# Performance work log

Measured on AMD Instinct MI355X. Metric: run time of the kernel, lower is better.

Reference implementation:

```python
import jax, jax.numpy as jnp
import numpy as np

B, N, ITERS = 8, 4096, 10  # batch, neurons (self.size), async-update sweeps


def setup_inputs() -> dict:
    key = jax.random.key(0)
    k1, k2, k3 = jax.random.split(key, 3)
    # bipolar {-1,+1} query patterns
    x = jnp.sign(jax.random.normal(k1, (B, N), dtype=jnp.float32))
    x = jnp.where(x == 0, 1.0, x)
    # symmetric Hebbian-style weight matrix with zero diagonal (as produced by fit())
    A = jax.random.normal(k2, (N, N), dtype=jnp.float32) / N
    W = 0.5 * (A + A.T)
    W = W - jnp.diag(jnp.diag(W))
    # one random neuron-visit permutation per (sample, sweep), replacing random.shuffle
    perm_keys = jax.random.split(k3, B * ITERS)
    perms = jax.vmap(lambda k: jax.random.permutation(k, N))(perm_keys)
    perms = perms.reshape(B, ITERS, N).astype(jnp.int32)
    return {"x": x, "weights": W, "perms": perms}


def reference(x, weights, perms):
    """Asynchronous Hopfield update: for each sample, sweep ITERS times over a
    random permutation of neurons, setting y[i] = sign(W[i] . y) sequentially."""
    flat_perms = perms.reshape(perms.shape[0], -1)  # [B, ITERS*N]

    def single(y0, perm_flat):
        def step(y, i):
            z = jnp.dot(weights[i], y)  # length-N dot, depends on previous updates
            return y.at[i].set(jnp.sign(z)), None
        y, _ = jax.lax.scan(step, y0, perm_flat)
        return y

    return jax.vmap(single)(x, flat_perms)  # [B, N]
```

## Files before the change

kernel.cpp:

```cpp
#include <hip/hip_runtime.h>

#define N 4096
#define B 8
#define ITERS 10
#define T (ITERS * N)
#define NT 256
#define E 16
#define WIN 1024
#define INFK 0xFFFFFFFFu
#define LIMIT 0x01000000u

__device__ __forceinline__ void lds_barrier() {
    asm volatile("s_waitcnt lgkmcnt(0)\n\ts_barrier" ::: "memory");
}

__global__ __launch_bounds__(256) void z0_gemv(const float* __restrict__ W,
                                               const float* __restrict__ x,
                                               double* __restrict__ Z0) {
    const int i = blockIdx.x;
    const int tid = threadIdx.x;
    const int lane = tid & 63;
    const int wid = tid >> 6;
    const float4* __restrict__ row = (const float4*)(W + (size_t)i * N);
    const float4* __restrict__ xv = (const float4*)x;

    double acc[B];
#pragma unroll
    for (int b = 0; b < B; ++b) acc[b] = 0.0;

#pragma unroll
    for (int it = 0; it < 4; ++it) {
        const int c = tid + 256 * it;
        const float4 w = row[c];
#pragma unroll
        for (int b = 0; b < B; ++b) {
            const float4 xb = xv[b * (N / 4) + c];
            acc[b] += (double)w.x * (double)xb.x + (double)w.y * (double)xb.y +
                      (double)w.z * (double)xb.z + (double)w.w * (double)xb.w;
        }
    }

#pragma unroll
    for (int off = 32; off > 0; off >>= 1) {
#pragma unroll
        for (int b = 0; b < B; ++b) acc[b] += __shfl_down(acc[b], off, 64);
    }

    __shared__ double red[4][B];
    if (lane == 0) {
#pragma unroll
        for (int b = 0; b < B; ++b) red[wid][b] = acc[b];
    }
    __syncthreads();
    if (tid < B)
        Z0[(size_t)tid * N + i] = red[0][tid] + red[1][tid] + red[2][tid] + red[3][tid];
}

__device__ __forceinline__ unsigned umin2(unsigned a, unsigned b) { return a < b ? a : b; }

template <int CTRL>
__device__ __forceinline__ unsigned dpp_min(unsigned v) {
    const int t = __builtin_amdgcn_update_dpp((int)v, (int)v, CTRL, 0xF, 0xF, false);
    return umin2(v, (unsigned)t);
}

__device__ __forceinline__ unsigned wave_min64(unsigned v) {
    v = dpp_min<0x111>(v);
    v = dpp_min<0x112>(v);
    v = dpp_min<0x114>(v);
    v = dpp_min<0x118>(v);
    v = dpp_min<0x142>(v);
    v = dpp_min<0x143>(v);
    return (unsigned)__builtin_amdgcn_readlane((int)v, 63);
}

__device__ __forceinline__ void fetch_row(const float* __restrict__ W, int i,
                                          int tid, float* wr) {
    const float4* __restrict__ rp = (const float4*)(W + (size_t)i * N) + 4 * tid;
    const float4 a = rp[0], c = rp[1], e = rp[2], f = rp[3];
    wr[0] = a.x;  wr[1] = a.y;  wr[2] = a.z;  wr[3] = a.w;
    wr[4] = c.x;  wr[5] = c.y;  wr[6] = c.z;  wr[7] = c.w;
    wr[8] = e.x;  wr[9] = e.y;  wr[10] = e.z; wr[11] = e.w;
    wr[12] = f.x; wr[13] = f.y; wr[14] = f.z; wr[15] = f.w;
}

__global__ __launch_bounds__(256) void hop_seq(const float* __restrict__ W,
                                               const float* __restrict__ x,
                                               const int* __restrict__ perms,
                                               const double* __restrict__ Z0,
                                               float* __restrict__ out) {
    const int b = blockIdx.x;
    const int tid = threadIdx.x;
    const int wid = tid >> 6;
    const int lane = tid & 63;

    __shared__ int wpos[N];
    __shared__ __align__(16) unsigned aP1[2][4];
    __shared__ __align__(16) unsigned aP2[2][4];
    __shared__ __align__(16) unsigned aV[2][4];

    double zj[E], zm[E];
    unsigned ym[E];
    unsigned sk[E];
    {
        const double* __restrict__ zsrc = Z0 + (size_t)b * N + E * tid;
#pragma unroll
        for (int k = 0; k < E; ++k) zj[k] = zsrc[k];
        const float4* __restrict__ xs = (const float4*)(x + (size_t)b * N);
#pragma unroll
        for (int q = 0; q < 4; ++q) {
            const float4 xv = xs[4 * tid + q];
            ym[4 * q + 0] = (xv.x > 0.f) ? 0xFFFFFFFFu : 0x7FFFFFFFu;
            ym[4 * q + 1] = (xv.y > 0.f) ? 0xFFFFFFFFu : 0x7FFFFFFFu;
            ym[4 * q + 2] = (xv.z > 0.f) ? 0xFFFFFFFFu : 0x7FFFFFFFu;
            ym[4 * q + 3] = (xv.w > 0.f) ? 0xFFFFFFFFu : 0x7FFFFFFFu;
        }
    }
    {
        const int4 z4 = make_int4(0, 0, 0, 0);
#pragma unroll
        for (int q = 0; q < 4; ++q) ((int4*)wpos)[tid + 256 * q] = z4;
    }
    lds_barrier();

    const int* __restrict__ perm_b = perms + (size_t)b * T;
    unsigned r = 0;

    for (int base = 0; base < T; base += WIN) {
        const int epoch = (base >> 10) + 1;
        const int4 iv = ((const int4*)(perm_b + base))[tid];
        wpos[iv.x] = (epoch << 10) | (4 * tid + 0);
        wpos[iv.y] = (epoch << 10) | (4 * tid + 1);
        wpos[iv.z] = (epoch << 10) | (4 * tid + 2);
        wpos[iv.w] = (epoch << 10) | (4 * tid + 3);
        lds_barrier();
#pragma unroll
        for (int q = 0; q < 4; ++q) {
            const int4 wp = ((const int4*)wpos)[4 * tid + q];
            const int e0 = 4 * q;
            const unsigned i0 = (unsigned)(E * tid + e0);
            sk[e0 + 0] = ((wp.x >> 10) == epoch)
                ? (((unsigned)(wp.x & 1023) << 14) | ((i0 + 0) << 2) | ((ym[e0 + 0] >> 30) & 2u)) : INFK;
            sk[e0 + 1] = ((wp.y >> 10) == epoch)
                ? (((unsigned)(wp.y & 1023) << 14) | ((i0 + 1) << 2) | ((ym[e0 + 1] >> 30) & 2u)) : INFK;
            sk[e0 + 2] = ((wp.z >> 10) == epoch)
                ? (((unsigned)(wp.z & 1023) << 14) | ((i0 + 2) << 2) | ((ym[e0 + 2] >> 30) & 2u)) : INFK;
            sk[e0 + 3] = ((wp.w >> 10) == epoch)
                ? (((unsigned)(wp.w & 1023) << 14) | ((i0 + 3) << 2) | ((ym[e0 + 3] >> 30) & 2u)) : INFK;
        }

        unsigned f1 = 0, f2v = 0;
        unsigned awk1 = 0, awk2 = 0;
        unsigned ckR = 0;
        float w1[E], w2[E];

        for (;;) {
            unsigned ckP, ckM = 0, gspan = 0;
            int i1 = 0, i2 = 0;
            double d1 = 0.0, d2 = 0.0;
            if (f1) {
                i1 = (int)((awk1 >> 2) & 4095u);
                d1 = (double)(-2 * ((int)(awk1 & 3u) - 1));
                if (f2v) {
                    i2 = (int)((awk2 >> 2) & 4095u);
                    d2 = (double)(-2 * ((int)(awk2 & 3u) - 1));
                    ckM = ((awk1 >> 14) + 1u) << 14;
                    ckP = ((awk2 >> 14) + 1u) << 14;
                    gspan = ckP - ckM;
                    if (tid == (i2 >> 4)) {
                        const int kk = i2 & 15;
#pragma unroll
                        for (int k = 0; k < E; ++k)
                            if (k == kk) { ym[k] ^= 0x80000000u; sk[k] ^= 2u; }
                    }
                } else {
                    ckP = ((awk1 >> 14) + 1u) << 14;
                }
                if (tid == (i1 >> 4)) {
                    const int kk = i1 & 15;
#pragma unroll
                    for (int k = 0; k < E; ++k)
                        if (k == kk) { ym[k] ^= 0x80000000u; sk[k] ^= 2u; }
                }
            } else {
                ckP = ckR;
            }

            unsigned keyP = INFK, vmin = INFK;
            if (f2v) {
#pragma unroll
                for (int k = 0; k < E; ++k) {
                    const double a = fma(d1, (double)w1[k], zj[k]);
                    zm[k] = a;
                    const unsigned tm = ((unsigned)__double2hiint(a)) ^ ym[k];
                    const unsigned cM = sk[k] | (unsigned)(((int)tm) >> 31);
                    vmin = umin2(vmin, cM - ckM);
                    const double c = fma(d2, (double)w2[k], a);
                    zj[k] = c;
                    const unsigned tp = ((unsigned)__double2hiint(c)) ^ ym[k];
                    keyP = umin2(keyP, (sk[k] | (unsigned)(((int)tp) >> 31)) - ckP);
                }
            } else if (f1) {
#pragma unroll
                for (int k = 0; k < E; ++k) {
                    const double c = fma(d1, (double)w1[k], zj[k]);
                    zj[k] = c;
                    const unsigned tp = ((unsigned)__double2hiint(c)) ^ ym[k];
                    keyP = umin2(keyP, (sk[k] | (unsigned)(((int)tp) >> 31)) - ckP);
                }
            } else {
#pragma unroll
                for (int k = 0; k < E; ++k) {
                    const unsigned tp = ((unsigned)__double2hiint(zj[k])) ^ ym[k];
                    keyP = umin2(keyP, (sk[k] | (unsigned)(((int)tp) >> 31)) - ckP);
                }
            }

            const unsigned m1 = wave_min64(keyP);
            const unsigned mv = f2v ? wave_min64(vmin) : INFK;
            const unsigned m2 = wave_min64(keyP == m1 ? INFK : keyP);

            const unsigned p = r & 1u; ++r;
            if (lane == 0) { aP1[p][wid] = m1; aP2[p][wid] = m2; aV[p][wid] = mv; }
            lds_barrier();
            const uint4 P1 = *(const uint4*)&aP1[p][0];
            const unsigned gP = umin2(umin2(P1.x, P1.y), umin2(P1.z, P1.w));
            if (f2v) {
                const uint4 V4 = *(const uint4*)&aV[p][0];
                const unsigned gV = umin2(umin2(V4.x, V4.y), umin2(V4.z, V4.w));
                if (gV < gspan) {
#pragma unroll
                    for (int k = 0; k < E; ++k) zj[k] = zm[k];
                    if (tid == (i2 >> 4)) {
                        const int kk = i2 & 15;
#pragma unroll
                        for (int k = 0; k < E; ++k)
                            if (k == kk) { ym[k] ^= 0x80000000u; sk[k] ^= 2u; }
                    }
                    const unsigned vabs = gV + ckM;
                    if ((vabs >> 14) == (awk2 >> 14)) {
                        f1 = 0; f2v = 0; ckR = ckM;
                    } else {
                        awk1 = vabs; f1 = 1; f2v = 0;
                        fetch_row(W, (int)((awk1 >> 2) & 4095u), tid, w1);
                    }
                    continue;
                }
            }
            if (gP >= LIMIT) break;
            awk1 = gP + ckP; f1 = 1;
            fetch_row(W, (int)((awk1 >> 2) & 4095u), tid, w1);
            const uint4 P2 = *(const uint4*)&aP2[p][0];
            const unsigned o0 = (P1.x == gP) ? P2.x : P1.x;
            const unsigned o1 = (P1.y == gP) ? P2.y : P1.y;
            const unsigned o2 = (P1.z == gP) ? P2.z : P1.z;
            const unsigned o3 = (P1.w == gP) ? P2.w : P1.w;
            const unsigned gP2 = umin2(umin2(o0, o1), umin2(o2, o3));
            f2v = (gP2 < LIMIT) ? 1u : 0u;
            if (f2v) {
                awk2 = gP2 + ckP;
                fetch_row(W, (int)((awk2 >> 2) & 4095u), tid, w2);
            }
        }
    }

    float4* __restrict__ os = (float4*)(out + (size_t)b * N);
#pragma unroll
    for (int q = 0; q < 4; ++q) {
        float4 o;
        o.x = (ym[4 * q + 0] & 0x80000000u) ? 1.0f : -1.0f;
        o.y = (ym[4 * q + 1] & 0x80000000u) ? 1.0f : -1.0f;
        o.z = (ym[4 * q + 2] & 0x80000000u) ? 1.0f : -1.0f;
        o.w = (ym[4 * q + 3] & 0x80000000u) ? 1.0f : -1.0f;
        os[4 * tid + q] = o;
    }
}

extern "C" void kernel_launch(void* const* d_in, const int* in_sizes, int n_in,
                              void* d_out, int out_size, void* d_ws, size_t ws_size,
                              hipStream_t stream) {
    const float* x = (const float*)d_in[0];
    const float* W = (const float*)d_in[1];
    const int* perms = (const int*)d_in[2];
    float* out = (float*)d_out;
    double* Z0 = (double*)d_ws;

    hipLaunchKernelGGL(z0_gemv, dim3(N), dim3(256), 0, stream, W, x, Z0);
    hipLaunchKernelGGL(hop_seq, dim3(B), dim3(NT), 0, stream, W, x, perms, Z0, out);
}
```

Baseline: 2.324 ms.

## Deepen speculative flip batching from two to four candidates per barrier round

Each barrier round now takes up to four lowest-key flip candidates instead of two. It applies their row updates in sequence and validates each speculative step with extra wave-min reductions, rolling back to the first point where an earlier neuron would flip. The aim is to cut the number of block-wide barrier and reduction rounds in the sequential async sweep. The cost is more row fetches, more FMA work and more reductions per round, higher register pressure (two extra weight rows held in registers), and wasted work when speculation fails.

After: 2.640 ms. +13.6%, slower.

```diff
diff --git a/kernel.cpp b/kernel.cpp
--- a/kernel.cpp
+++ b/kernel.cpp
@@ -57,6 +57,9 @@
 }
 
 __device__ __forceinline__ unsigned umin2(unsigned a, unsigned b) { return a < b ? a : b; }
+__device__ __forceinline__ unsigned umin4(unsigned a, unsigned b, unsigned c, unsigned d) {
+    return umin2(umin2(a, b), umin2(c, d));
+}
 
 template <int CTRL>
 __device__ __forceinline__ unsigned dpp_min(unsigned v) {
@@ -84,22 +87,31 @@
     wr[12] = f.x; wr[13] = f.y; wr[14] = f.z; wr[15] = f.w;
 }
 
-__global__ __launch_bounds__(256) void hop_seq(const float* __restrict__ W,
-                                               const float* __restrict__ x,
-                                               const int* __restrict__ perms,
-                                               const double* __restrict__ Z0,
-                                               float* __restrict__ out) {
+#define FIXUP(ii)                                                         \
+    do {                                                                  \
+        if (tid == ((ii) >> 4)) {                                         \
+            const int kk = (ii) & 15;                                     \
+            _Pragma("unroll") for (int k = 0; k < E; ++k) if (k == kk) {  \
+                ym[k] ^= 0x80000000u;                                     \
+                sk[k] ^= 2u;                                              \
+            }                                                             \
+        }                                                                 \
+    } while (0)
+
+__global__ __launch_bounds__(256, 1) void hop_seq(const float* __restrict__ W,
+                                                  const float* __restrict__ x,
+                                                  const int* __restrict__ perms,
+                                                  const double* __restrict__ Z0,
+                                                  float* __restrict__ out) {
     const int b = blockIdx.x;
     const int tid = threadIdx.x;
     const int wid = tid >> 6;
     const int lane = tid & 63;
 
     __shared__ int wpos[N];
-    __shared__ __align__(16) unsigned aP1[2][4];
-    __shared__ __align__(16) unsigned aP2[2][4];
-    __shared__ __align__(16) unsigned aV[2][4];
-
-    double zj[E], zm[E];
+    __shared__ __align__(16) unsigned pub[2][5][4];
+
+    double zj[E], zc[E];
     unsigned ym[E];
     unsigned sk[E];
     {
@@ -149,117 +161,198 @@
                 ? (((unsigned)(wp.w & 1023) << 14) | ((i0 + 3) << 2) | ((ym[e0 + 3] >> 30) & 2u)) : INFK;
         }
 
-        unsigned f1 = 0, f2v = 0;
-        unsigned awk1 = 0, awk2 = 0;
+        unsigned n = 0;
+        unsigned wk1 = 0, wk2 = 0, wk3 = 0, wk4 = 0;
         unsigned ckR = 0;
-        float w1[E], w2[E];
+        float w1[E], w2[E], w3[E], w4[E];
 
         for (;;) {
-            unsigned ckP, ckM = 0, gspan = 0;
-            int i1 = 0, i2 = 0;
-            double d1 = 0.0, d2 = 0.0;
-            if (f1) {
-                i1 = (int)((awk1 >> 2) & 4095u);
-                d1 = (double)(-2 * ((int)(awk1 & 3u) - 1));
-                if (f2v) {
-                    i2 = (int)((awk2 >> 2) & 4095u);
-                    d2 = (double)(-2 * ((int)(awk2 & 3u) - 1));
-                    ckM = ((awk1 >> 14) + 1u) << 14;
-                    ckP = ((awk2 >> 14) + 1u) << 14;
-                    gspan = ckP - ckM;
-                    if (tid == (i2 >> 4)) {
-                        const int kk = i2 & 15;
-#pragma unroll
-                        for (int k = 0; k < E; ++k)
-                            if (k == kk) { ym[k] ^= 0x80000000u; sk[k] ^= 2u; }
-                    }
-                } else {
-                    ckP = ((awk1 >> 14) + 1u) << 14;
-                }
-                if (tid == (i1 >> 4)) {
-                    const int kk = i1 & 15;
-#pragma unroll
-                    for (int k = 0; k < E; ++k)
-                        if (k == kk) { ym[k] ^= 0x80000000u; sk[k] ^= 2u; }
+            unsigned ck1 = 0, ck2 = 0, ck3 = 0, ck4 = 0, ckP;
+            int i1 = 0, i2 = 0, i3 = 0, i4 = 0;
+            double d1 = 0.0, d2 = 0.0, d3 = 0.0, d4 = 0.0;
+            if (n >= 1) {
+                i1 = (int)((wk1 >> 2) & 4095u);
+                d1 = (double)(-2 * ((int)(wk1 & 3u) - 1));
+                ck1 = ((wk1 >> 14) + 1u) << 14;
+                FIXUP(i1);
+            }
+            if (n >= 2) {
+                i2 = (int)((wk2 >> 2) & 4095u);
+                d2 = (double)(-2 * ((int)(wk2 & 3u) - 1));
+                ck2 = ((wk2 >> 14) + 1u) << 14;
+                FIXUP(i2);
+            }
+            if (n >= 3) {
+                i3 = (int)((wk3 >> 2) & 4095u);
+                d3 = (double)(-2 * ((int)(wk3 & 3u) - 1));
+                ck3 = ((wk3 >> 14) + 1u) << 14;
+                FIXUP(i3);
+            }
+            if (n >= 4) {
+                i4 = (int)((wk4 >> 2) & 4095u);
+                d4 = (double)(-2 * ((int)(wk4 & 3u) - 1));
+                ck4 = ((wk4 >> 14) + 1u) << 14;
+                FIXUP(i4);
+            }
+            ckP = (n == 0) ? ckR : (n == 1) ? ck1 : (n == 2) ? ck2 : (n == 3) ? ck3 : ck4;
+
+            unsigned key1 = INFK, key2 = INFK, key3 = INFK, keyP = INFK;
+            if (n == 0) {
+#pragma unroll
+                for (int k = 0; k < E; ++k) {
+                    const unsigned t = ((unsigned)__double2hiint(zj[k])) ^ ym[k];
+                    keyP = umin2(keyP, (sk[k] | (unsigned)(((int)t) >> 31)) - ckR);
                 }
             } else {
-                ckP = ckR;
-            }
-
-            unsigned keyP = INFK, vmin = INFK;
-            if (f2v) {
 #pragma unroll
                 for (int k = 0; k < E; ++k) {
                     const double a = fma(d1, (double)w1[k], zj[k]);
-                    zm[k] = a;
-                    const unsigned tm = ((unsigned)__double2hiint(a)) ^ ym[k];
-                    const unsigned cM = sk[k] | (unsigned)(((int)tm) >> 31);
-                    vmin = umin2(vmin, cM - ckM);
-                    const double c = fma(d2, (double)w2[k], a);
-                    zj[k] = c;
-                    const unsigned tp = ((unsigned)__double2hiint(c)) ^ ym[k];
-                    keyP = umin2(keyP, (sk[k] | (unsigned)(((int)tp) >> 31)) - ckP);
-                }
-            } else if (f1) {
-#pragma unroll
-                for (int k = 0; k < E; ++k) {
-                    const double c = fma(d1, (double)w1[k], zj[k]);
-                    zj[k] = c;
-                    const unsigned tp = ((unsigned)__double2hiint(c)) ^ ym[k];
-                    keyP = umin2(keyP, (sk[k] | (unsigned)(((int)tp) >> 31)) - ckP);
-                }
-            } else {
-#pragma unroll
-                for (int k = 0; k < E; ++k) {
-                    const unsigned tp = ((unsigned)__double2hiint(zj[k])) ^ ym[k];
-                    keyP = umin2(keyP, (sk[k] | (unsigned)(((int)tp) >> 31)) - ckP);
+                    zc[k] = a;
+                    const unsigned t = ((unsigned)__double2hiint(a)) ^ ym[k];
+                    key1 = umin2(key1, (sk[k] | (unsigned)(((int)t) >> 31)) - ck1);
+                }
+                if (n == 1) {
+#pragma unroll
+                    for (int k = 0; k < E; ++k) zj[k] = zc[k];
+                    keyP = key1;
+                }
+                if (n >= 2) {
+#pragma unroll
+                    for (int k = 0; k < E; ++k) {
+                        const double c = fma(d2, (double)w2[k], zc[k]);
+                        zj[k] = c;
+                        const unsigned t = ((unsigned)__double2hiint(c)) ^ ym[k];
+                        key2 = umin2(key2, (sk[k] | (unsigned)(((int)t) >> 31)) - ck2);
+                    }
+                    if (n == 2) keyP = key2;
+                }
+                if (n >= 3) {
+#pragma unroll
+                    for (int k = 0; k < E; ++k) {
+                        const double c = fma(d3, (double)w3[k], zj[k]);
+                        zj[k] = c;
+                        const unsigned t = ((unsigned)__double2hiint(c)) ^ ym[k];
+                        key3 = umin2(key3, (sk[k] | (unsigned)(((int)t) >> 31)) - ck3);
+                    }
+                    if (n == 3) keyP = key3;
+                }
+                if (n >= 4) {
+                    unsigned key4 = INFK;
+#pragma unroll
+                    for (int k = 0; k < E; ++k) {
+                        const double c = fma(d4, (double)w4[k], zj[k]);
+                        zj[k] = c;
+                        const unsigned t = ((unsigned)__double2hiint(c)) ^ ym[k];
+                        key4 = umin2(key4, (sk[k] | (unsigned)(((int)t) >> 31)) - ck4);
+                    }
+                    keyP = key4;
                 }
             }
 
             const unsigned m1 = wave_min64(keyP);
-            const unsigned mv = f2v ? wave_min64(vmin) : INFK;
+            const unsigned mv1 = (n >= 2) ? wave_min64(key1) : INFK;
+            const unsigned mv2 = (n >= 3) ? wave_min64(key2) : INFK;
+            const unsigned mv3 = (n >= 4) ? wave_min64(key3) : INFK;
             const unsigned m2 = wave_min64(keyP == m1 ? INFK : keyP);
 
+            unsigned pv = m1;
+            pv = (lane == 1) ? m2 : pv;
+            pv = (lane == 2) ? mv1 : pv;
+            pv = (lane == 3) ? mv2 : pv;
+            pv = (lane == 4) ? mv3 : pv;
             const unsigned p = r & 1u; ++r;
-            if (lane == 0) { aP1[p][wid] = m1; aP2[p][wid] = m2; aV[p][wid] = mv; }
+            if (lane < 5) pub[p][lane][wid] = pv;
             lds_barrier();
-            const uint4 P1 = *(const uint4*)&aP1[p][0];
-            const unsigned gP = umin2(umin2(P1.x, P1.y), umin2(P1.z, P1.w));
-            if (f2v) {
-                const uint4 V4 = *(const uint4*)&aV[p][0];
-                const unsigned gV = umin2(umin2(V4.x, V4.y), umin2(V4.z, V4.w));
-                if (gV < gspan) {
-#pragma unroll
-                    for (int k = 0; k < E; ++k) zj[k] = zm[k];
-                    if (tid == (i2 >> 4)) {
-                        const int kk = i2 & 15;
-#pragma unroll
-                        for (int k = 0; k < E; ++k)
-                            if (k == kk) { ym[k] ^= 0x80000000u; sk[k] ^= 2u; }
+
+            const uint4 M1 = *(const uint4*)&pub[p][0][0];
+            const uint4 M2 = *(const uint4*)&pub[p][1][0];
+
+            if (n >= 2) {
+                const uint4 V1 = *(const uint4*)&pub[p][2][0];
+                const unsigned gv1 = umin4(V1.x, V1.y, V1.z, V1.w);
+                if (gv1 < ck2 - ck1) {
+#pragma unroll
+                    for (int k = 0; k < E; ++k) zj[k] = zc[k];
+                    FIXUP(i2);
+                    if (n >= 3) FIXUP(i3);
+                    if (n >= 4) FIXUP(i4);
+                    const unsigned vabs = gv1 + ck1;
+                    if ((vabs >> 14) == (wk2 >> 14)) { n = 0; ckR = ck2; }
+                    else { wk1 = vabs; n = 1; fetch_row(W, (int)((vabs >> 2) & 4095u), tid, w1); }
+                    continue;
+                }
+            }
+            if (n >= 3) {
+                const uint4 V2 = *(const uint4*)&pub[p][3][0];
+                const unsigned gv2 = umin4(V2.x, V2.y, V2.z, V2.w);
+                if (gv2 < ck3 - ck2) {
+#pragma unroll
+                    for (int k = 0; k < E; ++k) zj[k] = fma(d2, (double)w2[k], zc[k]);
+                    FIXUP(i3);
+                    if (n >= 4) FIXUP(i4);
+                    const unsigned vabs = gv2 + ck2;
+                    if ((vabs >> 14) == (wk3 >> 14)) { n = 0; ckR = ck3; }
+                    else { wk1 = vabs; n = 1; fetch_row(W, (int)((vabs >> 2) & 4095u), tid, w1); }
+                    continue;
+                }
+            }
+            if (n >= 4) {
+                const uint4 V3 = *(const uint4*)&pub[p][4][0];
+                const unsigned gv3 = umin4(V3.x, V3.y, V3.z, V3.w);
+                if (gv3 < ck4 - ck3) {
+#pragma unroll
+                    for (int k = 0; k < E; ++k)
+                        zj[k] = fma(d3, (double)w3[k], fma(d2, (double)w2[k], zc[k]));
+                    FIXUP(i4);
+                    const unsigned vabs = gv3 + ck3;
+                    if ((vabs >> 14) == (wk4 >> 14)) { n = 0; ckR = ck4; }
+                    else { wk1 = vabs; n = 1; fetch_row(W, (int)((vabs >> 2) & 4095u), tid, w1); }
+                    continue;
+                }
+            }
+
+            unsigned h0 = M1.x, h1 = M1.y, h2 = M1.z, h3 = M1.w;
+            unsigned x0 = M2.x, x1 = M2.y, x2 = M2.z, x3 = M2.w;
+            const unsigned g1 = umin4(h0, h1, h2, h3);
+            if (g1 >= LIMIT) break;
+            {
+                const bool c0 = (h0 == g1), c1 = (h1 == g1), c2 = (h2 == g1), c3 = (h3 == g1);
+                h0 = c0 ? x0 : h0; x0 = c0 ? INFK : x0;
+                h1 = c1 ? x1 : h1; x1 = c1 ? INFK : x1;
+                h2 = c2 ? x2 : h2; x2 = c2 ? INFK : x2;
+                h3 = c3 ? x3 : h3; x3 = c3 ? INFK : x3;
+            }
+            const unsigned g2 = umin4(h0, h1, h2, h3);
+            {
+                const bool c0 = (h0 == g2), c1 = (h1 == g2), c2 = (h2 == g2), c3 = (h3 == g2);
+                h0 = c0 ? x0 : h0; x0 = c0 ? INFK : x0;
+                h1 = c1 ? x1 : h1; x1 = c1 ? INFK : x1;
+                h2 = c2 ? x2 : h2; x2 = c2 ? INFK : x2;
+                h3 = c3 ? x3 : h3; x3 = c3 ? INFK : x3;
+            }
+            const unsigned g3 = umin4(h0, h1, h2, h3);
+            {
+                const bool c0 = (h0 == g3), c1 = (h1 == g3), c2 = (h2 == g3), c3 = (h3 == g3);
+                h0 = c0 ? x0 : h0;
+                h1 = c1 ? x1 : h1;
+                h2 = c2 ? x2 : h2;
+                h3 = c3 ? x3 : h3;
+            }
+            const unsigned g4 = umin4(h0, h1, h2, h3);
+
+            wk1 = g1 + ckP; n = 1;
+            fetch_row(W, (int)((wk1 >> 2) & 4095u), tid, w1);
+            if (g2 < LIMIT) {
+                wk2 = g2 + ckP; n = 2;
+                fetch_row(W, (int)((wk2 >> 2) & 4095u), tid, w2);
+                if (g3 < LIMIT) {
+                    wk3 = g3 + ckP; n = 3;
+                    fetch_row(W, (int)((wk3 >> 2) & 4095u), tid, w3);
+                    if (g4 < LIMIT) {
+                        wk4 = g4 + ckP; n = 4;
+                        fetch_row(W, (int)((wk4 >> 2) & 4095u), tid, w4);
                     }
-                    const unsigned vabs = gV + ckM;
-                    if ((vabs >> 14) == (awk2 >> 14)) {
-                        f1 = 0; f2v = 0; ckR = ckM;
-                    } else {
-                        awk1 = vabs; f1 = 1; f2v = 0;
-                        fetch_row(W, (int)((awk1 >> 2) & 4095u), tid, w1);
-                    }
-                    continue;
-                }
-            }
-            if (gP >= LIMIT) break;
-            awk1 = gP + ckP; f1 = 1;
-            fetch_row(W, (int)((awk1 >> 2) & 4095u), tid, w1);
-            const uint4 P2 = *(const uint4*)&aP2[p][0];
-            const unsigned o0 = (P1.x == gP) ? P2.x : P1.x;
-            const unsigned o1 = (P1.y == gP) ? P2.y : P1.y;
-            const unsigned o2 = (P1.z == gP) ? P2.z : P1.z;
-            const unsigned o3 = (P1.w == gP) ? P2.w : P1.w;
-            const unsigned gP2 = umin2(umin2(o0, o1), umin2(o2, o3));
-            f2v = (gP2 < LIMIT) ? 1u : 0u;
-            if (f2v) {
-                awk2 = gP2 + ckP;
-                fetch_row(W, (int)((awk2 >> 2) & 4095u), tid, w2);
+                }
             }
         }
     }
```

## Replace triple wave-min reductions with quarter-wave DPP mins and speculative row prefetch

Applied to the files above, without the earlier changes.

The per-step reduction is reworked. The three full wave reductions (min, second-min, validation) become one 16-lane quarter-wave DPP min published as 16 LDS candidates plus one full-wave min for validation, which drops the readlane calls. The first-min and second-min are then derived from the 16 published values, and the next row fetch is issued before the validation check is resolved. The z0_gemv kernel is also changed to process two rows per block, reusing each x load, and hop_seq gets launch_bounds(256,1). The goal is to shorten the serial critical path of each sequential update step, at the cost of some wasted speculative fetches.

Result: faster. 2.216 ms (-4.6%).

```diff
diff --git a/kernel.cpp b/kernel.cpp
--- a/kernel.cpp
+++ b/kernel.cpp
@@ -17,46 +17,60 @@
 __global__ __launch_bounds__(256) void z0_gemv(const float* __restrict__ W,
                                                const float* __restrict__ x,
                                                double* __restrict__ Z0) {
-    const int i = blockIdx.x;
+    const int i0 = 2 * blockIdx.x;
     const int tid = threadIdx.x;
     const int lane = tid & 63;
     const int wid = tid >> 6;
-    const float4* __restrict__ row = (const float4*)(W + (size_t)i * N);
+    const float4* __restrict__ row0 = (const float4*)(W + (size_t)i0 * N);
+    const float4* __restrict__ row1 = (const float4*)(W + (size_t)(i0 + 1) * N);
     const float4* __restrict__ xv = (const float4*)x;
 
-    double acc[B];
-#pragma unroll
-    for (int b = 0; b < B; ++b) acc[b] = 0.0;
+    double acc0[B], acc1[B];
+#pragma unroll
+    for (int b = 0; b < B; ++b) { acc0[b] = 0.0; acc1[b] = 0.0; }
 
 #pragma unroll
     for (int it = 0; it < 4; ++it) {
         const int c = tid + 256 * it;
-        const float4 w = row[c];
+        const float4 w0 = row0[c];
+        const float4 w1 = row1[c];
 #pragma unroll
         for (int b = 0; b < B; ++b) {
             const float4 xb = xv[b * (N / 4) + c];
-            acc[b] += (double)w.x * (double)xb.x + (double)w.y * (double)xb.y +
-                      (double)w.z * (double)xb.z + (double)w.w * (double)xb.w;
+            acc0[b] += (double)w0.x * (double)xb.x + (double)w0.y * (double)xb.y +
+                       (double)w0.z * (double)xb.z + (double)w0.w * (double)xb.w;
+            acc1[b] += (double)w1.x * (double)xb.x + (double)w1.y * (double)xb.y +
+                       (double)w1.z * (double)xb.z + (double)w1.w * (double)xb.w;
         }
     }
 
 #pragma unroll
     for (int off = 32; off > 0; off >>= 1) {
 #pragma unroll
-        for (int b = 0; b < B; ++b) acc[b] += __shfl_down(acc[b], off, 64);
-    }
-
-    __shared__ double red[4][B];
+        for (int b = 0; b < B; ++b) {
+            acc0[b] += __shfl_down(acc0[b], off, 64);
+            acc1[b] += __shfl_down(acc1[b], off, 64);
+        }
+    }
+
+    __shared__ double red[4][2][B];
     if (lane == 0) {
 #pragma unroll
-        for (int b = 0; b < B; ++b) red[wid][b] = acc[b];
+        for (int b = 0; b < B; ++b) { red[wid][0][b] = acc0[b]; red[wid][1][b] = acc1[b]; }
     }
     __syncthreads();
-    if (tid < B)
-        Z0[(size_t)tid * N + i] = red[0][tid] + red[1][tid] + red[2][tid] + red[3][tid];
+    if (tid < B) {
+        Z0[(size_t)tid * N + i0] =
+            red[0][0][tid] + red[1][0][tid] + red[2][0][tid] + red[3][0][tid];
+        Z0[(size_t)tid * N + i0 + 1] =
+            red[0][1][tid] + red[1][1][tid] + red[2][1][tid] + red[3][1][tid];
+    }
 }
 
 __device__ __forceinline__ unsigned umin2(unsigned a, unsigned b) { return a < b ? a : b; }
+__device__ __forceinline__ unsigned umin4(unsigned a, unsigned b, unsigned c, unsigned d) {
+    return umin2(umin2(a, b), umin2(c, d));
+}
 
 template <int CTRL>
 __device__ __forceinline__ unsigned dpp_min(unsigned v) {
@@ -64,14 +78,19 @@
     return umin2(v, (unsigned)t);
 }
 
-__device__ __forceinline__ unsigned wave_min64(unsigned v) {
+__device__ __forceinline__ unsigned quarter_min(unsigned v) {
     v = dpp_min<0x111>(v);
     v = dpp_min<0x112>(v);
     v = dpp_min<0x114>(v);
     v = dpp_min<0x118>(v);
+    return v;
+}
+
+__device__ __forceinline__ unsigned full_min(unsigned v) {
+    v = quarter_min(v);
     v = dpp_min<0x142>(v);
     v = dpp_min<0x143>(v);
-    return (unsigned)__builtin_amdgcn_readlane((int)v, 63);
+    return v;
 }
 
 __device__ __forceinline__ void fetch_row(const float* __restrict__ W, int i,
@@ -84,22 +103,32 @@
     wr[12] = f.x; wr[13] = f.y; wr[14] = f.z; wr[15] = f.w;
 }
 
-__global__ __launch_bounds__(256) void hop_seq(const float* __restrict__ W,
-                                               const float* __restrict__ x,
-                                               const int* __restrict__ perms,
-                                               const double* __restrict__ Z0,
-                                               float* __restrict__ out) {
+#define FIXUP(ii)                                                         \
+    do {                                                                  \
+        if (tid == ((ii) >> 4)) {                                         \
+            const int kk = (ii) & 15;                                     \
+            _Pragma("unroll") for (int k = 0; k < E; ++k) if (k == kk) {  \
+                ym[k] ^= 0x80000000u;                                     \
+                sk[k] ^= 2u;                                              \
+            }                                                             \
+        }                                                                 \
+    } while (0)
+
+__global__ __launch_bounds__(256, 1) void hop_seq(const float* __restrict__ W,
+                                                  const float* __restrict__ x,
+                                                  const int* __restrict__ perms,
+                                                  const double* __restrict__ Z0,
+                                                  float* __restrict__ out) {
     const int b = blockIdx.x;
     const int tid = threadIdx.x;
     const int wid = tid >> 6;
     const int lane = tid & 63;
 
     __shared__ int wpos[N];
-    __shared__ __align__(16) unsigned aP1[2][4];
-    __shared__ __align__(16) unsigned aP2[2][4];
-    __shared__ __align__(16) unsigned aV[2][4];
-
-    double zj[E], zm[E];
+    __shared__ __align__(16) unsigned pubP[2][16];
+    __shared__ __align__(16) unsigned pubV[2][4];
+
+    double zj[E], zc[E];
     unsigned ym[E];
     unsigned sk[E];
     {
@@ -149,117 +178,121 @@
                 ? (((unsigned)(wp.w & 1023) << 14) | ((i0 + 3) << 2) | ((ym[e0 + 3] >> 30) & 2u)) : INFK;
         }
 
-        unsigned f1 = 0, f2v = 0;
-        unsigned awk1 = 0, awk2 = 0;
+        unsigned n = 0;
+        unsigned wk1 = 0, wk2 = 0;
         unsigned ckR = 0;
         float w1[E], w2[E];
 
         for (;;) {
-            unsigned ckP, ckM = 0, gspan = 0;
+            unsigned ck1 = 0, ck2 = 0, ckP;
             int i1 = 0, i2 = 0;
             double d1 = 0.0, d2 = 0.0;
-            if (f1) {
-                i1 = (int)((awk1 >> 2) & 4095u);
-                d1 = (double)(-2 * ((int)(awk1 & 3u) - 1));
-                if (f2v) {
-                    i2 = (int)((awk2 >> 2) & 4095u);
-                    d2 = (double)(-2 * ((int)(awk2 & 3u) - 1));
-                    ckM = ((awk1 >> 14) + 1u) << 14;
-                    ckP = ((awk2 >> 14) + 1u) << 14;
-                    gspan = ckP - ckM;
-                    if (tid == (i2 >> 4)) {
-                        const int kk = i2 & 15;
-#pragma unroll
-                        for (int k = 0; k < E; ++k)
-                            if (k == kk) { ym[k] ^= 0x80000000u; sk[k] ^= 2u; }
-                    }
-                } else {
-                    ckP = ((awk1 >> 14) + 1u) << 14;
-                }
-                if (tid == (i1 >> 4)) {
-                    const int kk = i1 & 15;
-#pragma unroll
-                    for (int k = 0; k < E; ++k)
-                        if (k == kk) { ym[k] ^= 0x80000000u; sk[k] ^= 2u; }
-                }
-            } else {
-                ckP = ckR;
-            }
-
-            unsigned keyP = INFK, vmin = INFK;
-            if (f2v) {
+            if (n >= 1) {
+                i1 = (int)((wk1 >> 2) & 4095u);
+                d1 = (double)(-2 * ((int)(wk1 & 3u) - 1));
+                ck1 = ((wk1 >> 14) + 1u) << 14;
+                FIXUP(i1);
+            }
+            if (n == 2) {
+                i2 = (int)((wk2 >> 2) & 4095u);
+                d2 = (double)(-2 * ((int)(wk2 & 3u) - 1));
+                ck2 = ((wk2 >> 14) + 1u) << 14;
+                FIXUP(i2);
+            }
+            ckP = (n == 0) ? ckR : (n == 1) ? ck1 : ck2;
+
+            unsigned key1 = INFK, keyP = INFK;
+            if (n == 2) {
 #pragma unroll
                 for (int k = 0; k < E; ++k) {
                     const double a = fma(d1, (double)w1[k], zj[k]);
-                    zm[k] = a;
+                    zc[k] = a;
                     const unsigned tm = ((unsigned)__double2hiint(a)) ^ ym[k];
-                    const unsigned cM = sk[k] | (unsigned)(((int)tm) >> 31);
-                    vmin = umin2(vmin, cM - ckM);
+                    key1 = umin2(key1, (sk[k] | (unsigned)(((int)tm) >> 31)) - ck1);
                     const double c = fma(d2, (double)w2[k], a);
                     zj[k] = c;
                     const unsigned tp = ((unsigned)__double2hiint(c)) ^ ym[k];
-                    keyP = umin2(keyP, (sk[k] | (unsigned)(((int)tp) >> 31)) - ckP);
+                    keyP = umin2(keyP, (sk[k] | (unsigned)(((int)tp) >> 31)) - ck2);
                 }
-            } else if (f1) {
+            } else if (n == 1) {
 #pragma unroll
                 for (int k = 0; k < E; ++k) {
                     const double c = fma(d1, (double)w1[k], zj[k]);
                     zj[k] = c;
                     const unsigned tp = ((unsigned)__double2hiint(c)) ^ ym[k];
-                    keyP = umin2(keyP, (sk[k] | (unsigned)(((int)tp) >> 31)) - ckP);
+                    keyP = umin2(keyP, (sk[k] | (unsigned)(((int)tp) >> 31)) - ck1);
                 }
             } else {
 #pragma unroll
                 for (int k = 0; k < E; ++k) {
                     const unsigned tp = ((unsigned)__double2hiint(zj[k])) ^ ym[k];
-                    keyP = umin2(keyP, (sk[k] | (unsigned)(((int)tp) >> 31)) - ckP);
+                    keyP = umin2(keyP, (sk[k] | (unsigned)(((int)tp) >> 31)) - ckR);
                 }
             }
 
-            const unsigned m1 = wave_min64(keyP);
-            const unsigned mv = f2v ? wave_min64(vmin) : INFK;
-            const unsigned m2 = wave_min64(keyP == m1 ? INFK : keyP);
+            const unsigned vP = quarter_min(keyP);
+            const unsigned vV = full_min(key1);
 
             const unsigned p = r & 1u; ++r;
-            if (lane == 0) { aP1[p][wid] = m1; aP2[p][wid] = m2; aV[p][wid] = mv; }
+            if ((lane & 15) == 15) pubP[p][4 * wid + (lane >> 4)] = vP;
+            if (lane == 63) pubV[p][wid] = vV;
             lds_barrier();
-            const uint4 P1 = *(const uint4*)&aP1[p][0];
-            const unsigned gP = umin2(umin2(P1.x, P1.y), umin2(P1.z, P1.w));
-            if (f2v) {
-                const uint4 V4 = *(const uint4*)&aV[p][0];
-                const unsigned gV = umin2(umin2(V4.x, V4.y), umin2(V4.z, V4.w));
-                if (gV < gspan) {
-#pragma unroll
-                    for (int k = 0; k < E; ++k) zj[k] = zm[k];
-                    if (tid == (i2 >> 4)) {
-                        const int kk = i2 & 15;
-#pragma unroll
-                        for (int k = 0; k < E; ++k)
-                            if (k == kk) { ym[k] ^= 0x80000000u; sk[k] ^= 2u; }
-                    }
-                    const unsigned vabs = gV + ckM;
-                    if ((vabs >> 14) == (awk2 >> 14)) {
-                        f1 = 0; f2v = 0; ckR = ckM;
+
+            const uint4 q0 = *(const uint4*)&pubP[p][0];
+            const uint4 q1 = *(const uint4*)&pubP[p][4];
+            const uint4 q2 = *(const uint4*)&pubP[p][8];
+            const uint4 q3 = *(const uint4*)&pubP[p][12];
+            const unsigned g1 = umin2(umin2(umin4(q0.x, q0.y, q0.z, q0.w),
+                                            umin4(q1.x, q1.y, q1.z, q1.w)),
+                                      umin2(umin4(q2.x, q2.y, q2.z, q2.w),
+                                            umin4(q3.x, q3.y, q3.z, q3.w)));
+            if (g1 < LIMIT)
+                fetch_row(W, (int)(((g1 + ckP) >> 2) & 4095u), tid, w1);
+
+            const unsigned a00 = (q0.x == g1) ? INFK : q0.x;
+            const unsigned a01 = (q0.y == g1) ? INFK : q0.y;
+            const unsigned a02 = (q0.z == g1) ? INFK : q0.z;
+            const unsigned a03 = (q0.w == g1) ? INFK : q0.w;
+            const unsigned a10 = (q1.x == g1) ? INFK : q1.x;
+            const unsigned a11 = (q1.y == g1) ? INFK : q1.y;
+            const unsigned a12 = (q1.z == g1) ? INFK : q1.z;
+            const unsigned a13 = (q1.w == g1) ? INFK : q1.w;
+            const unsigned a20 = (q2.x == g1) ? INFK : q2.x;
+            const unsigned a21 = (q2.y == g1) ? INFK : q2.y;
+            const unsigned a22 = (q2.z == g1) ? INFK : q2.z;
+            const unsigned a23 = (q2.w == g1) ? INFK : q2.w;
+            const unsigned a30 = (q3.x == g1) ? INFK : q3.x;
+            const unsigned a31 = (q3.y == g1) ? INFK : q3.y;
+            const unsigned a32 = (q3.z == g1) ? INFK : q3.z;
+            const unsigned a33 = (q3.w == g1) ? INFK : q3.w;
+            const unsigned g2 = umin2(umin2(umin4(a00, a01, a02, a03),
+                                            umin4(a10, a11, a12, a13)),
+                                      umin2(umin4(a20, a21, a22, a23),
+                                            umin4(a30, a31, a32, a33)));
+
+            if (n == 2) {
+                const uint4 vv = *(const uint4*)&pubV[p][0];
+                const unsigned gv = umin4(vv.x, vv.y, vv.z, vv.w);
+                if (gv < ck2 - ck1) {
+#pragma unroll
+                    for (int k = 0; k < E; ++k) zj[k] = zc[k];
+                    FIXUP(i2);
+                    const unsigned vabs = gv + ck1;
+                    if ((vabs >> 14) == (wk2 >> 14)) {
+                        n = 0; ckR = ck2;
                     } else {
-                        awk1 = vabs; f1 = 1; f2v = 0;
-                        fetch_row(W, (int)((awk1 >> 2) & 4095u), tid, w1);
+                        wk1 = vabs;
+                        fetch_row(W, (int)((vabs >> 2) & 4095u), tid, w1);
                     }
                     continue;
                 }
             }
-            if (gP >= LIMIT) break;
-            awk1 = gP + ckP; f1 = 1;
-            fetch_row(W, (int)((awk1 >> 2) & 4095u), tid, w1);
-            const uint4 P2 = *(const uint4*)&aP2[p][0];
-            const unsigned o0 = (P1.x == gP) ? P2.x : P1.x;
-            const unsigned o1 = (P1.y == gP) ? P2.y : P1.y;
-            const unsigned o2 = (P1.z == gP) ? P2.z : P1.z;
-            const unsigned o3 = (P1.w == gP) ? P2.w : P1.w;
-            const unsigned gP2 = umin2(umin2(o0, o1), umin2(o2, o3));
-            f2v = (gP2 < LIMIT) ? 1u : 0u;
-            if (f2v) {
-                awk2 = gP2 + ckP;
-                fetch_row(W, (int)((awk2 >> 2) & 4095u), tid, w2);
+
+            if (g1 >= LIMIT) break;
+            wk1 = g1 + ckP; n = 1;
+            if (g2 < LIMIT) {
+                wk2 = g2 + ckP; n = 2;
+                fetch_row(W, (int)((wk2 >> 2) & 4095u), tid, w2);
             }
         }
     }
@@ -285,6 +318,6 @@
     float* out = (float*)d_out;
     double* Z0 = (double*)d_ws;
 
-    hipLaunchKernelGGL(z0_gemv, dim3(N), dim3(256), 0, stream, W, x, Z0);
+    hipLaunchKernelGGL(z0_gemv, dim3(N / 2), dim3(256), 0, stream, W, x, Z0);
     hipLaunchKernelGGL(hop_seq, dim3(B), dim3(NT), 0, stream, W, x, perms, Z0, out);
 }
```
